# Optimization experiments

Measured on AMD Instinct MI355X. Metric: run time of the kernel, lower is better.

## Reference

```python
import jax, jax.numpy as jnp
import numpy as np

B, S, H = 2, 2048, 1024          # batch, seq, hidden_size
I = 512                          # expert_ffn_hidden_size
E_R, E_Z = 32, 8                 # routed experts, zero (identity) experts
E_T = E_R + E_Z                  # total experts
K = 6                            # moe_topk
SCALE = 2.5                      # routed_scaling_factor
W_INIT = 0.02


def setup_inputs() -> dict:
    key = jax.random.key(0)
    k0, k1, k2, k3 = jax.random.split(key, 4)
    return {
        "hidden_states": jax.random.normal(k0, (B, S, H), jnp.float32),
        "classifier_weight": jax.random.normal(k1, (E_T, H), jnp.float32) * W_INIT,
        "e_score_correction_bias": jnp.zeros((E_T,), jnp.float32),
        "gate_up_proj": jax.random.normal(k2, (E_T, 2 * I, H), jnp.float32) * W_INIT,
        "down_proj": jax.random.normal(k3, (E_R, H, I), jnp.float32) * W_INIT,
    }


def reference(hidden_states, classifier_weight, e_score_correction_bias,
              gate_up_proj, down_proj):
    orig_shape = hidden_states.shape
    x = hidden_states.reshape(-1, H).astype(jnp.float32)      # [T, H]
    T = x.shape[0]

    # ---- router (fp32 like the torch code) ----
    logits = x @ classifier_weight.T                          # [T, E_T]
    scores = jax.nn.softmax(logits, axis=-1)
    _, topk_idx = jax.lax.top_k(scores + e_score_correction_bias[None, :], K)
    topk_w = jnp.take_along_axis(scores, topk_idx, axis=1) * SCALE  # [T, K]

    # dense per-(token, expert) combine weights; 0 for unselected experts
    w_full = jnp.zeros((T, E_T), jnp.float32).at[
        jnp.arange(T)[:, None], topk_idx].add(topk_w)          # [T, E_T]

    # zero experts: weighted identity
    zero_w = w_full[:, E_R:].sum(axis=-1, keepdims=True)       # [T, 1]
    out0 = x * zero_w

    # routed experts: SwiGLU MLP per expert, scanned over experts
    routed_w = w_full[:, :E_R].T                               # [E_R, T]

    def body(out, xs):
        Wgu, Wd, we = xs                                       # [2I,H],[H,I],[T]
        gate, up = jnp.split(x @ Wgu.T, 2, axis=-1)            # [T, I] each
        y = (jax.nn.silu(gate) * up) @ Wd.T                    # [T, H]
        return out + we[:, None] * y, None

    out, _ = jax.lax.scan(body, out0, (gate_up_proj[:E_R], down_proj, routed_w))
    return out.reshape(orig_shape).astype(hidden_states.dtype)
```

## Files before the change

kernel.cpp:

```cpp
#include <hip/hip_runtime.h>
#include <float.h>
#include <math.h>

#define TT 4096
#define HH 1024
#define II 512
#define E_R 32
#define E_T 40
#define TOPK 6
#define SCALE_F 2.5f
#define MAXTILES 224
#define NGUP (32*1024*1024)
#define NDWN (32*1024*512)

typedef __bf16 bf16x8 __attribute__((ext_vector_type(8)));
typedef float f32x4 __attribute__((ext_vector_type(4)));

__device__ inline unsigned short f2bf(float f) {
  __bf16 h = (__bf16)f;
  return __builtin_bit_cast(unsigned short, h);
}

__device__ inline bf16x8 cvt8v(float4 a, float4 b) {
  bf16x8 v;
  v[0] = (__bf16)a.x; v[1] = (__bf16)a.y; v[2] = (__bf16)a.z; v[3] = (__bf16)a.w;
  v[4] = (__bf16)b.x; v[5] = (__bf16)b.y; v[6] = (__bf16)b.z; v[7] = (__bf16)b.w;
  return v;
}

__device__ inline void gload_lds16(const void* g, void* l) {
  __builtin_amdgcn_global_load_lds(
      (__attribute__((address_space(1))) void*)g,
      (__attribute__((address_space(3))) void*)l, 16, 0, 0);
}

__device__ inline bf16x8 lds_frag(const unsigned short* base, int row, int kb) {
  int byte = (row * 128 + kb * 2) ^ ((row & 7) << 4);
  uint4 v = *reinterpret_cast<const uint4*>(reinterpret_cast<const char*>(base) + byte);
  return __builtin_bit_cast(bf16x8, v);
}

__device__ inline f32x4 mfma16(bf16x8 a, bf16x8 b, f32x4 c) {
  return __builtin_amdgcn_mfma_f32_16x16x32_bf16(a, b, c, 0, 0, 0);
}

__global__ __launch_bounds__(256) void k_convert_w(const float* __restrict__ gup,
                                                   const float* __restrict__ dwn,
                                                   uint4* __restrict__ wb) {
  unsigned i = blockIdx.x * 256 + threadIdx.x;
  const unsigned NGq = NGUP / 8;
  const float4* src = (i < NGq)
      ? reinterpret_cast<const float4*>(gup) + (size_t)i * 2
      : reinterpret_cast<const float4*>(dwn) + (size_t)(i - NGq) * 2;
  float4 a = src[0], b = src[1];
  wb[i] = __builtin_bit_cast(uint4, cvt8v(a, b));
}

__global__ __launch_bounds__(256) void k_logits(const float* __restrict__ x,
                                                const float* __restrict__ wcls,
                                                float* __restrict__ logits,
                                                unsigned short* __restrict__ xb) {
  __shared__ float4 ws4[E_T * 64];
  const int tid = threadIdx.x;
  const int lane = tid & 63;
  const int wave = tid >> 6;
  const int token = blockIdx.x * 4 + wave;
  const float4* x4 = reinterpret_cast<const float4*>(x);
  const float4* w4 = reinterpret_cast<const float4*>(wcls);

  float acc[E_T];
  #pragma unroll
  for (int e = 0; e < E_T; ++e) acc[e] = 0.f;

  for (int c = 0; c < 4; ++c) {
    if (c) __syncthreads();
    #pragma unroll
    for (int j = 0; j < 10; ++j) {
      int v = tid + j * 256;
      int e = v >> 6, kq = v & 63;
      ws4[v] = w4[e * 256 + c * 64 + kq];
    }
    float4 xv = x4[(size_t)token * 256 + c * 64 + lane];
    ushort4 s;
    s.x = f2bf(xv.x); s.y = f2bf(xv.y); s.z = f2bf(xv.z); s.w = f2bf(xv.w);
    reinterpret_cast<ushort4*>(xb + (size_t)token * HH)[c * 64 + lane] = s;
    __syncthreads();
    #pragma unroll
    for (int e = 0; e < E_T; ++e) {
      float4 w = ws4[e * 64 + lane];
      acc[e] += xv.x * w.x + xv.y * w.y + xv.z * w.z + xv.w * w.w;
    }
  }

  float mine = 0.f;
  #pragma unroll
  for (int e = 0; e < E_T; ++e) {
    float r = acc[e];
    #pragma unroll
    for (int o = 32; o; o >>= 1) r += __shfl_xor(r, o);
    if (lane == e) mine = r;
  }
  if (lane < E_T) logits[(size_t)token * E_T + lane] = mine;
}

__global__ void k_topk(const float* __restrict__ logits, const float* __restrict__ bias,
                       float* __restrict__ zero_w, int* __restrict__ counts,
                       int* __restrict__ tok_list,
                       int* __restrict__ route_ep, float* __restrict__ route_w,
                       int* __restrict__ route_n) {
  int t = blockIdx.x * 64 + threadIdx.x;
  float l[E_T];
  const float4* lp = reinterpret_cast<const float4*>(logits + (size_t)t * E_T);
  #pragma unroll
  for (int j = 0; j < E_T / 4; ++j) {
    float4 v = lp[j];
    l[j * 4 + 0] = v.x; l[j * 4 + 1] = v.y; l[j * 4 + 2] = v.z; l[j * 4 + 3] = v.w;
  }
  float m = -FLT_MAX;
  #pragma unroll
  for (int e = 0; e < E_T; ++e) m = fmaxf(m, l[e]);
  float den = 0.f;
  #pragma unroll
  for (int e = 0; e < E_T; ++e) { l[e] = __expf(l[e] - m); den += l[e]; }
  float inv = 1.f / den;
  float sel[E_T];
  #pragma unroll
  for (int e = 0; e < E_T; ++e) { l[e] *= inv; sel[e] = l[e] + bias[e]; }

  unsigned long long used = 0ull;
  float zw = 0.f;
  int nr = 0;
  for (int k = 0; k < TOPK; ++k) {
    float bv = -FLT_MAX; int bj = 0;
    #pragma unroll
    for (int e = 0; e < E_T; ++e) {
      float v = ((used >> e) & 1ull) ? -FLT_MAX : sel[e];
      if (v > bv) { bv = v; bj = e; }
    }
    used |= 1ull << bj;
    float wgt = (bv - bias[bj]) * SCALE_F;
    if (bj >= E_R) {
      zw += wgt;
    } else {
      int p = atomicAdd(&counts[bj], 1);
      tok_list[bj * TT + p] = t;
      route_ep[t * TOPK + nr] = (bj << 16) | p;
      route_w[t * TOPK + nr] = wgt;
      nr++;
    }
  }
  zero_w[t] = zw;
  route_n[t] = nr;
}

__global__ void k_scan(const int* __restrict__ counts, int* __restrict__ offsets,
                       int* __restrict__ tiles) {
  if (threadIdx.x == 0) {
    int s = 0, idx = 0;
    for (int e = 0; e < E_R; ++e) {
      offsets[e] = s;
      int c = counts[e];
      s += c;
      for (int r0 = 0; r0 < c; r0 += 128) tiles[1 + idx++] = (e << 16) | r0;
    }
    offsets[E_R] = s;
    tiles[0] = idx;
  }
}

__global__ __launch_bounds__(256, 3) void k_gemm1(
    const unsigned short* __restrict__ xb, const unsigned short* __restrict__ gupb,
    const int* __restrict__ tok_list, const int* __restrict__ counts,
    const int* __restrict__ offsets, const int* __restrict__ tiles,
    unsigned short* __restrict__ inter) {
  const int nt = tiles[0];
  if ((int)blockIdx.y >= nt) return;
  const int tv = tiles[1 + blockIdx.y];
  const int e = tv >> 16;
  const int row0 = tv & 0xffff;
  const int cnt = counts[e];
  const int off = offsets[e];
  const int n0 = blockIdx.x * 64;
  const int tid = threadIdx.x;
  const int lane = tid & 63;
  const int wave = tid >> 6;
  const int wr = wave >> 1;
  const int wc = wave & 1;

  __shared__ __align__(16) unsigned short lA[2][128 * 64];
  __shared__ __align__(16) unsigned short lBg[2][64 * 64];
  __shared__ __align__(16) unsigned short lBu[2][64 * 64];
  __shared__ int toks[128];

  if (tid < 128) {
    int r = row0 + tid;
    toks[tid] = tok_list[e * TT + (r < cnt ? r : cnt - 1)];
  }
  __syncthreads();

  unsigned aoff[4];
  #pragma unroll
  for (int i = 0; i < 4; ++i) {
    int lrow = wave * 32 + i * 8 + (lane >> 3);
    aoff[i] = (unsigned)toks[lrow] * HH + (((lane & 7) ^ (lrow & 7)) * 8);
  }
  const unsigned short* gb = gupb + (size_t)e * (1024 * HH);
  unsigned boff[2];
  #pragma unroll
  for (int i = 0; i < 2; ++i) {
    int lrow = wave * 16 + i * 8 + (lane >> 3);
    boff[i] = (unsigned)(n0 + lrow) * HH + (((lane & 7) ^ (lrow & 7)) * 8);
  }
  const unsigned upjump = 512u * HH;

  f32x4 accg[4][2] = {}; f32x4 accu[4][2] = {};

#define G1_STAGE(T, B)                                                          \
  {                                                                             \
    int k0s = (T) * 64;                                                         \
    _Pragma("unroll")                                                           \
    for (int i = 0; i < 4; ++i)                                                 \
      gload_lds16(xb + aoff[i] + k0s, lA[B] + (wave * 32 + i * 8) * 64);        \
    _Pragma("unroll")                                                           \
    for (int i = 0; i < 2; ++i) {                                               \
      gload_lds16(gb + boff[i] + k0s,          lBg[B] + (wave * 16 + i * 8) * 64); \
      gload_lds16(gb + boff[i] + upjump + k0s, lBu[B] + (wave * 16 + i * 8) * 64); \
    }                                                                           \
  }

  G1_STAGE(0, 0);
  __syncthreads();

  for (int t = 0; t < 16; ++t) {
    if (t < 15) {
      if ((t + 1) & 1) { G1_STAGE(t + 1, 1); } else { G1_STAGE(t + 1, 0); }
    }
    const unsigned short* cA  = (t & 1) ? lA[1]  : lA[0];
    const unsigned short* cBg = (t & 1) ? lBg[1] : lBg[0];
    const unsigned short* cBu = (t & 1) ? lBu[1] : lBu[0];
    #pragma unroll
    for (int ks = 0; ks < 2; ++ks) {
      int kb = ks * 32 + ((lane >> 4) << 3);
      bf16x8 a[4], g[2], u[2];
      #pragma unroll
      for (int i = 0; i < 4; ++i) a[i] = lds_frag(cA, wr * 64 + i * 16 + (lane & 15), kb);
      #pragma unroll
      for (int j = 0; j < 2; ++j) {
        g[j] = lds_frag(cBg, wc * 32 + j * 16 + (lane & 15), kb);
        u[j] = lds_frag(cBu, wc * 32 + j * 16 + (lane & 15), kb);
      }
      #pragma unroll
      for (int i = 0; i < 4; ++i)
        #pragma unroll
        for (int j = 0; j < 2; ++j) {
          accg[i][j] = mfma16(a[i], g[j], accg[i][j]);
          accu[i][j] = mfma16(a[i], u[j], accu[i][j]);
        }
    }
    __syncthreads();
  }

  #pragma unroll
  for (int i = 0; i < 4; ++i)
    #pragma unroll
    for (int j = 0; j < 2; ++j)
      #pragma unroll
      for (int r = 0; r < 4; ++r) {
        int rloc = wr * 64 + i * 16 + ((lane >> 4) << 2) + r;
        int grow = row0 + rloc;
        if (grow < cnt) {
          int col = n0 + wc * 32 + j * 16 + (lane & 15);
          float gv = accg[i][j][r], uv = accu[i][j][r];
          float act = gv / (1.f + __expf(-gv)) * uv;
          inter[(size_t)(off + grow) * II + col] = f2bf(act);
        }
      }
}

__global__ __launch_bounds__(256, 3) void k_gemm2(
    const unsigned short* __restrict__ inter, const unsigned short* __restrict__ dwnb,
    const int* __restrict__ counts, const int* __restrict__ offsets,
    const int* __restrict__ tiles, unsigned short* __restrict__ inter2) {
  const int nt = tiles[0];
  if ((int)blockIdx.y >= nt) return;
  const int tv = tiles[1 + blockIdx.y];
  const int e = tv >> 16;
  const int row0 = tv & 0xffff;
  const int cnt = counts[e];
  const int off = offsets[e];
  const int h0 = blockIdx.x * 128;
  const int tid = threadIdx.x;
  const int lane = tid & 63;
  const int wave = tid >> 6;
  const int wr = wave >> 1;
  const int wc = wave & 1;

  __shared__ __align__(16) unsigned short lA[2][128 * 64];
  __shared__ __align__(16) unsigned short lB[2][128 * 64];

  unsigned aoff[4];
  #pragma unroll
  for (int i = 0; i < 4; ++i) {
    int lrow = wave * 32 + i * 8 + (lane >> 3);
    int rr = row0 + lrow; rr = rr < cnt ? rr : cnt - 1;
    aoff[i] = (unsigned)(off + rr) * II + (((lane & 7) ^ (lrow & 7)) * 8);
  }
  const unsigned short* db = dwnb + (size_t)e * (HH * II);
  unsigned boff[4];
  #pragma unroll
  for (int i = 0; i < 4; ++i) {
    int lrow = wave * 32 + i * 8 + (lane >> 3);
    boff[i] = (unsigned)(h0 + lrow) * II + (((lane & 7) ^ (lrow & 7)) * 8);
  }

  f32x4 acc[4][4] = {};

#define G2_STAGE(T, B)                                                          \
  {                                                                             \
    int k0s = (T) * 64;                                                         \
    _Pragma("unroll")                                                           \
    for (int i = 0; i < 4; ++i)                                                 \
      gload_lds16(inter + aoff[i] + k0s, lA[B] + (wave * 32 + i * 8) * 64);     \
    _Pragma("unroll")                                                           \
    for (int i = 0; i < 4; ++i)                                                 \
      gload_lds16(db + boff[i] + k0s, lB[B] + (wave * 32 + i * 8) * 64);        \
  }

  G2_STAGE(0, 0);
  __syncthreads();

  for (int t = 0; t < 8; ++t) {
    if (t < 7) {
      if ((t + 1) & 1) { G2_STAGE(t + 1, 1); } else { G2_STAGE(t + 1, 0); }
    }
    const unsigned short* cA = (t & 1) ? lA[1] : lA[0];
    const unsigned short* cB = (t & 1) ? lB[1] : lB[0];
    #pragma unroll
    for (int ks = 0; ks < 2; ++ks) {
      int kb = ks * 32 + ((lane >> 4) << 3);
      bf16x8 a[4], b[4];
      #pragma unroll
      for (int i = 0; i < 4; ++i) a[i] = lds_frag(cA, wr * 64 + i * 16 + (lane & 15), kb);
      #pragma unroll
      for (int j = 0; j < 4; ++j) b[j] = lds_frag(cB, wc * 64 + j * 16 + (lane & 15), kb);
      #pragma unroll
      for (int i = 0; i < 4; ++i)
        #pragma unroll
        for (int j = 0; j < 4; ++j)
          acc[i][j] = mfma16(a[i], b[j], acc[i][j]);
    }
    __syncthreads();
  }

  #pragma unroll
  for (int i = 0; i < 4; ++i)
    #pragma unroll
    for (int j = 0; j < 4; ++j)
      #pragma unroll
      for (int r = 0; r < 4; ++r) {
        int rloc = wr * 64 + i * 16 + ((lane >> 4) << 2) + r;
        int grow = row0 + rloc;
        if (grow < cnt) {
          int h = h0 + wc * 64 + j * 16 + (lane & 15);
          inter2[(size_t)(off + grow) * HH + h] = f2bf(acc[i][j][r]);
        }
      }
}

__global__ __launch_bounds__(256) void k_combine(
    const float* __restrict__ x, const float* __restrict__ zero_w,
    const int* __restrict__ offsets, const int* __restrict__ route_ep,
    const float* __restrict__ route_w, const int* __restrict__ route_n,
    const unsigned short* __restrict__ inter2, float* __restrict__ out) {
  const int t = blockIdx.x;
  const int tid = threadIdx.x;
  const float zw = zero_w[t];
  const int n = route_n[t];
  float4 o = reinterpret_cast<const float4*>(x)[t * 256 + tid];
  o.x *= zw; o.y *= zw; o.z *= zw; o.w *= zw;
  for (int i = 0; i < n; ++i) {
    int ep = route_ep[t * TOPK + i];
    int row = offsets[ep >> 16] + (ep & 0xffff);
    float w = route_w[t * TOPK + i];
    ushort4 v = reinterpret_cast<const ushort4*>(inter2 + (size_t)row * HH)[tid];
    o.x += w * __builtin_bit_cast(float, (unsigned)v.x << 16);
    o.y += w * __builtin_bit_cast(float, (unsigned)v.y << 16);
    o.z += w * __builtin_bit_cast(float, (unsigned)v.z << 16);
    o.w += w * __builtin_bit_cast(float, (unsigned)v.w << 16);
  }
  reinterpret_cast<float4*>(out)[t * 256 + tid] = o;
}


extern "C" void kernel_launch(void* const* d_in, const int* in_sizes, int n_in,
                              void* d_out, int out_size, void* d_ws, size_t ws_size,
                              hipStream_t stream) {
  const float* x    = (const float*)d_in[0];
  const float* wcls = (const float*)d_in[1];
  const float* bias = (const float*)d_in[2];
  const float* gup  = (const float*)d_in[3];
  const float* dwn  = (const float*)d_in[4];
  float* out = (float*)d_out;

  char* w = (char*)d_ws;
  unsigned short* xb    = (unsigned short*)(w + 0);
  float* zero_w         = (float*)(w + 8388608);
  int* counts           = (int*)(w + 8404992);
  int* offsets          = (int*)(w + 8405120);
  int* tok_list         = (int*)(w + 8405376);
  float* logits         = (float*)(w + 8929664);
  int* tiles            = (int*)(w + 9585024);
  int* route_ep         = (int*)(w + 9589120);
  float* route_w        = (float*)(w + 9687424);
  int* route_n          = (int*)(w + 9785728);
  unsigned short* inter = (unsigned short*)(w + 9802112);
  unsigned short* inter2 = (unsigned short*)(w + 34967936);
  unsigned short* gupb  = (unsigned short*)(w + 85299584);
  unsigned short* dwnb  = (unsigned short*)(w + 152408448);

  hipMemsetAsync(counts, 0, E_R * sizeof(int), stream);
  k_convert_w<<<(NGUP + NDWN) / 8 / 256, 256, 0, stream>>>(gup, dwn, (uint4*)gupb);
  k_logits<<<1024, 256, 0, stream>>>(x, wcls, logits, xb);
  k_topk<<<64, 64, 0, stream>>>(logits, bias, zero_w, counts, tok_list,
                                route_ep, route_w, route_n);
  k_scan<<<1, 64, 0, stream>>>(counts, offsets, tiles);
  k_gemm1<<<dim3(8, MAXTILES), 256, 0, stream>>>(xb, gupb, tok_list, counts, offsets, tiles, inter);
  k_gemm2<<<dim3(8, MAXTILES), 256, 0, stream>>>(inter, dwnb, counts, offsets, tiles, inter2);
  k_combine<<<TT, 256, 0, stream>>>(x, zero_w, offsets, route_ep, route_w, route_n,
                                    inter2, out);
}
```

Before: 262.9 us.

## Pipeline GEMM loads with explicit vmcnt waits and raw barriers; fold counts memset

Rewrites the main loops of both grouped GEMM kernels to keep two LDS stages in flight. Partial `s_waitcnt vmcnt(8)` waits, raw `s_barrier` calls and scheduling barriers replace `__syncthreads`, so the next tile's global-to-LDS loads overlap the MFMA compute. It also removes the separate memset of the expert counts and instead zeroes them inside the logits kernel, saving one launch. The hand-tuned waitcnt values depend on the exact number of loads issued per stage, and the manual barrier choreography is fragile if the stage contents change.

Result: faster. 247.6 us (-5.8%).

```diff
diff --git a/kernel.cpp b/kernel.cpp
--- a/kernel.cpp
+++ b/kernel.cpp
@@ -44,6 +44,11 @@
   return __builtin_amdgcn_mfma_f32_16x16x32_bf16(a, b, c, 0, 0, 0);
 }
 
+#define WAIT_VM8()  do { asm volatile("s_waitcnt vmcnt(8)" ::: "memory"); } while (0)
+#define WAIT_VM0()  do { asm volatile("s_waitcnt vmcnt(0)" ::: "memory"); } while (0)
+#define SBAR()      __builtin_amdgcn_s_barrier()
+#define SCHED0()    __builtin_amdgcn_sched_barrier(0)
+
 __global__ __launch_bounds__(256) void k_convert_w(const float* __restrict__ gup,
                                                    const float* __restrict__ dwn,
                                                    uint4* __restrict__ wb) {
@@ -59,12 +64,14 @@
 __global__ __launch_bounds__(256) void k_logits(const float* __restrict__ x,
                                                 const float* __restrict__ wcls,
                                                 float* __restrict__ logits,
-                                                unsigned short* __restrict__ xb) {
+                                                unsigned short* __restrict__ xb,
+                                                int* __restrict__ counts) {
   __shared__ float4 ws4[E_T * 64];
   const int tid = threadIdx.x;
   const int lane = tid & 63;
   const int wave = tid >> 6;
   const int token = blockIdx.x * 4 + wave;
+  if (blockIdx.x == 0 && tid < E_R) counts[tid] = 0;
   const float4* x4 = reinterpret_cast<const float4*>(x);
   const float4* w4 = reinterpret_cast<const float4*>(wcls);
 
@@ -228,37 +235,49 @@
     }                                                                           \
   }
 
+#define G1_COMPUTE(B)                                                           \
+  {                                                                             \
+    _Pragma("unroll")                                                           \
+    for (int ks = 0; ks < 2; ++ks) {                                            \
+      int kb = ks * 32 + ((lane >> 4) << 3);                                    \
+      bf16x8 a[4], g[2], u[2];                                                  \
+      _Pragma("unroll")                                                         \
+      for (int i = 0; i < 4; ++i) a[i] = lds_frag(lA[B], wr * 64 + i * 16 + (lane & 15), kb); \
+      _Pragma("unroll")                                                         \
+      for (int j = 0; j < 2; ++j) {                                             \
+        g[j] = lds_frag(lBg[B], wc * 32 + j * 16 + (lane & 15), kb);            \
+        u[j] = lds_frag(lBu[B], wc * 32 + j * 16 + (lane & 15), kb);            \
+      }                                                                         \
+      _Pragma("unroll")                                                         \
+      for (int i = 0; i < 4; ++i)                                               \
+        _Pragma("unroll")                                                       \
+        for (int j = 0; j < 2; ++j) {                                           \
+          accg[i][j] = mfma16(a[i], g[j], accg[i][j]);                          \
+          accu[i][j] = mfma16(a[i], u[j], accu[i][j]);                          \
+        }                                                                       \
+    }                                                                           \
+  }
+
   G1_STAGE(0, 0);
-  __syncthreads();
-
-  for (int t = 0; t < 16; ++t) {
-    if (t < 15) {
-      if ((t + 1) & 1) { G1_STAGE(t + 1, 1); } else { G1_STAGE(t + 1, 0); }
-    }
-    const unsigned short* cA  = (t & 1) ? lA[1]  : lA[0];
-    const unsigned short* cBg = (t & 1) ? lBg[1] : lBg[0];
-    const unsigned short* cBu = (t & 1) ? lBu[1] : lBu[0];
-    #pragma unroll
-    for (int ks = 0; ks < 2; ++ks) {
-      int kb = ks * 32 + ((lane >> 4) << 3);
-      bf16x8 a[4], g[2], u[2];
-      #pragma unroll
-      for (int i = 0; i < 4; ++i) a[i] = lds_frag(cA, wr * 64 + i * 16 + (lane & 15), kb);
-      #pragma unroll
-      for (int j = 0; j < 2; ++j) {
-        g[j] = lds_frag(cBg, wc * 32 + j * 16 + (lane & 15), kb);
-        u[j] = lds_frag(cBu, wc * 32 + j * 16 + (lane & 15), kb);
-      }
-      #pragma unroll
-      for (int i = 0; i < 4; ++i)
-        #pragma unroll
-        for (int j = 0; j < 2; ++j) {
-          accg[i][j] = mfma16(a[i], g[j], accg[i][j]);
-          accu[i][j] = mfma16(a[i], u[j], accu[i][j]);
-        }
-    }
-    __syncthreads();
-  }
+  G1_STAGE(1, 1);
+  WAIT_VM8();
+  SBAR(); SCHED0();
+
+  #pragma unroll 2
+  for (int t = 0; t < 14; ++t) {
+    if (t & 1) { G1_COMPUTE(1); } else { G1_COMPUTE(0); }
+    SCHED0();
+    SBAR();
+    if (t & 1) { G1_STAGE(t + 2, 1); } else { G1_STAGE(t + 2, 0); }
+    WAIT_VM8();
+    SBAR(); SCHED0();
+  }
+  G1_COMPUTE(0);
+  SCHED0();
+  SBAR();
+  WAIT_VM0();
+  SBAR(); SCHED0();
+  G1_COMPUTE(1);
 
   #pragma unroll
   for (int i = 0; i < 4; ++i)
@@ -326,31 +345,44 @@
       gload_lds16(db + boff[i] + k0s, lB[B] + (wave * 32 + i * 8) * 64);        \
   }
 
+#define G2_COMPUTE(B)                                                           \
+  {                                                                             \
+    _Pragma("unroll")                                                           \
+    for (int ks = 0; ks < 2; ++ks) {                                            \
+      int kb = ks * 32 + ((lane >> 4) << 3);                                    \
+      bf16x8 a[4], b[4];                                                        \
+      _Pragma("unroll")                                                         \
+      for (int i = 0; i < 4; ++i) a[i] = lds_frag(lA[B], wr * 64 + i * 16 + (lane & 15), kb); \
+      _Pragma("unroll")                                                         \
+      for (int j = 0; j < 4; ++j) b[j] = lds_frag(lB[B], wc * 64 + j * 16 + (lane & 15), kb); \
+      _Pragma("unroll")                                                         \
+      for (int i = 0; i < 4; ++i)                                               \
+        _Pragma("unroll")                                                       \
+        for (int j = 0; j < 4; ++j)                                             \
+          acc[i][j] = mfma16(a[i], b[j], acc[i][j]);                            \
+    }                                                                           \
+  }
+
   G2_STAGE(0, 0);
-  __syncthreads();
-
-  for (int t = 0; t < 8; ++t) {
-    if (t < 7) {
-      if ((t + 1) & 1) { G2_STAGE(t + 1, 1); } else { G2_STAGE(t + 1, 0); }
-    }
-    const unsigned short* cA = (t & 1) ? lA[1] : lA[0];
-    const unsigned short* cB = (t & 1) ? lB[1] : lB[0];
-    #pragma unroll
-    for (int ks = 0; ks < 2; ++ks) {
-      int kb = ks * 32 + ((lane >> 4) << 3);
-      bf16x8 a[4], b[4];
-      #pragma unroll
-      for (int i = 0; i < 4; ++i) a[i] = lds_frag(cA, wr * 64 + i * 16 + (lane & 15), kb);
-      #pragma unroll
-      for (int j = 0; j < 4; ++j) b[j] = lds_frag(cB, wc * 64 + j * 16 + (lane & 15), kb);
-      #pragma unroll
-      for (int i = 0; i < 4; ++i)
-        #pragma unroll
-        for (int j = 0; j < 4; ++j)
-          acc[i][j] = mfma16(a[i], b[j], acc[i][j]);
-    }
-    __syncthreads();
-  }
+  G2_STAGE(1, 1);
+  WAIT_VM8();
+  SBAR(); SCHED0();
+
+  #pragma unroll 2
+  for (int t = 0; t < 6; ++t) {
+    if (t & 1) { G2_COMPUTE(1); } else { G2_COMPUTE(0); }
+    SCHED0();
+    SBAR();
+    if (t & 1) { G2_STAGE(t + 2, 1); } else { G2_STAGE(t + 2, 0); }
+    WAIT_VM8();
+    SBAR(); SCHED0();
+  }
+  G2_COMPUTE(0);
+  SCHED0();
+  SBAR();
+  WAIT_VM0();
+  SBAR(); SCHED0();
+  G2_COMPUTE(1);
 
   #pragma unroll
   for (int i = 0; i < 4; ++i)
@@ -418,9 +450,8 @@
   unsigned short* gupb  = (unsigned short*)(w + 85299584);
   unsigned short* dwnb  = (unsigned short*)(w + 152408448);
 
-  hipMemsetAsync(counts, 0, E_R * sizeof(int), stream);
   k_convert_w<<<(NGUP + NDWN) / 8 / 256, 256, 0, stream>>>(gup, dwn, (uint4*)gupb);
-  k_logits<<<1024, 256, 0, stream>>>(x, wcls, logits, xb);
+  k_logits<<<1024, 256, 0, stream>>>(x, wcls, logits, xb, counts);
   k_topk<<<64, 64, 0, stream>>>(logits, bias, zero_w, counts, tok_list,
                                 route_ep, route_w, route_n);
   k_scan<<<1, 64, 0, stream>>>(counts, offsets, tiles);
```
